# Kernel optimization log

Hardware: AMD Instinct MI355X
Metric: run time of the kernel (lower is better)

Reference implementation:

```python
import jax, jax.numpy as jnp
import numpy as np

B, N = 256, 100000

def setup_inputs() -> dict:
    key = jax.random.key(0)
    k1, k2 = jax.random.split(key)
    preds = jax.random.normal(k1, (B, N), dtype=jnp.float32)
    labels = jax.random.normal(k2, (B, N), dtype=jnp.float32)
    return {"preds": preds, "labels": labels, "subject": 0}

def reference(preds, labels, subject):
    # Batch-parallel Pearson: five fused row reductions instead of a Python loop.
    n = jnp.asarray(preds.shape[1], preds.dtype)
    sum_x = jnp.sum(preds, axis=1)
    sum_y = jnp.sum(labels, axis=1)
    sum_xy = jnp.sum(preds * labels, axis=1)
    sum_x2 = jnp.sum(preds * preds, axis=1)
    sum_y2 = jnp.sum(labels * labels, axis=1)
    num = n * sum_xy - sum_x * sum_y
    den = jnp.sqrt((n * sum_x2 - sum_x ** 2) * (n * sum_y2 - sum_y ** 2))
    pearson = num / den
    return jnp.mean(1.0 - pearson)
```

## Files before the change

kernel.cpp:

```cpp
#include <hip/hip_runtime.h>

#define B_ROWS   256
#define SPLIT    8
#define NTHREADS 256
#define NBLOCKS  (B_ROWS * SPLIT)


__global__ __launch_bounds__(NTHREADS) void pearson_partial(
    const float* __restrict__ preds,
    const float* __restrict__ labels,
    float* __restrict__ ws,
    int N)
{
    const int bid = blockIdx.x;
    const int row = bid >> 3;
    const int seg = bid & (SPLIT - 1);
    const int tid = threadIdx.x;

    const int n4      = N >> 2;
    const int per_seg = n4 / SPLIT;
    const int begin   = seg * per_seg;
    const int end     = begin + per_seg;

    const float4* p4 = reinterpret_cast<const float4*>(preds  + (size_t)row * N);
    const float4* l4 = reinterpret_cast<const float4*>(labels + (size_t)row * N);

    float sx = 0.f, sy = 0.f, sxy = 0.f, sxx = 0.f, syy = 0.f;

    for (int i = begin + tid; i < end; i += NTHREADS) {
        float4 a = p4[i];
        float4 b = l4[i];
        sx += a.x; sy += b.x; sxy = fmaf(a.x, b.x, sxy); sxx = fmaf(a.x, a.x, sxx); syy = fmaf(b.x, b.x, syy);
        sx += a.y; sy += b.y; sxy = fmaf(a.y, b.y, sxy); sxx = fmaf(a.y, a.y, sxx); syy = fmaf(b.y, b.y, syy);
        sx += a.z; sy += b.z; sxy = fmaf(a.z, b.z, sxy); sxx = fmaf(a.z, a.z, sxx); syy = fmaf(b.z, b.z, syy);
        sx += a.w; sy += b.w; sxy = fmaf(a.w, b.w, sxy); sxx = fmaf(a.w, a.w, sxx); syy = fmaf(b.w, b.w, syy);
    }

    for (int o = 32; o > 0; o >>= 1) {
        sx  += __shfl_down(sx,  o, 64);
        sy  += __shfl_down(sy,  o, 64);
        sxy += __shfl_down(sxy, o, 64);
        sxx += __shfl_down(sxx, o, 64);
        syy += __shfl_down(syy, o, 64);
    }

    __shared__ float red[4][5];
    const int wave = tid >> 6;
    const int lane = tid & 63;
    if (lane == 0) {
        red[wave][0] = sx;  red[wave][1] = sy;  red[wave][2] = sxy;
        red[wave][3] = sxx; red[wave][4] = syy;
    }
    __syncthreads();

    if (tid == 0) {
        ws[0 * NBLOCKS + bid] = red[0][0] + red[1][0] + red[2][0] + red[3][0];
        ws[1 * NBLOCKS + bid] = red[0][1] + red[1][1] + red[2][1] + red[3][1];
        ws[2 * NBLOCKS + bid] = red[0][2] + red[1][2] + red[2][2] + red[3][2];
        ws[3 * NBLOCKS + bid] = red[0][3] + red[1][3] + red[2][3] + red[3][3];
        ws[4 * NBLOCKS + bid] = red[0][4] + red[1][4] + red[2][4] + red[3][4];
    }
}

__global__ __launch_bounds__(NTHREADS) void pearson_final(
    const float* __restrict__ ws,
    float* __restrict__ out,
    int N)
{
    const int t = threadIdx.x;
    const float4* ws4 = reinterpret_cast<const float4*>(ws);

    float4 v[5][2];
#pragma unroll
    for (int j = 0; j < 5; ++j) {
        v[j][0] = ws4[j * (NBLOCKS / 4) + 2 * t];
        v[j][1] = ws4[j * (NBLOCKS / 4) + 2 * t + 1];
    }

    double acc[5];
#pragma unroll
    for (int j = 0; j < 5; ++j) {
        acc[j] = (double)v[j][0].x + (double)v[j][0].y + (double)v[j][0].z + (double)v[j][0].w
               + (double)v[j][1].x + (double)v[j][1].y + (double)v[j][1].z + (double)v[j][1].w;
    }

    const double n   = (double)N;
    const double num = n * acc[2] - acc[0] * acc[1];
    const double den = sqrt((n * acc[3] - acc[0] * acc[0]) * (n * acc[4] - acc[1] * acc[1]));
    double val = 1.0 - num / den;

    for (int o = 32; o > 0; o >>= 1)
        val += __shfl_down(val, o, 64);

    __shared__ double dred[4];
    const int wave = t >> 6;
    const int lane = t & 63;
    if (lane == 0) dred[wave] = val;
    __syncthreads();

    if (t == 0)
        out[0] = (float)((dred[0] + dred[1] + dred[2] + dred[3]) / (double)B_ROWS);
}

extern "C" void kernel_launch(void* const* d_in, const int* in_sizes, int n_in,
                              void* d_out, int out_size, void* d_ws, size_t ws_size,
                              hipStream_t stream)
{
    const float* preds  = (const float*)d_in[0];
    const float* labels = (const float*)d_in[1];

    const int N = in_sizes[0] / B_ROWS;

    float* ws  = (float*)d_ws;
    float* out = (float*)d_out;

    pearson_partial<<<NBLOCKS, NTHREADS, 0, stream>>>(preds, labels, ws, N);
    pearson_final<<<1, NTHREADS, 0, stream>>>(ws, out, N);
}
```

Measured before the change: 37.82 us.

## Fuse partial and final Pearson kernels into one row-per-block kernel with atomic output

Replaces the two-kernel scheme (8 blocks per row writing partials, then a single-block final reduction) with one kernel. Each 1024-thread block reduces a full row, computes that row's Pearson term in double, and atomically adds it into the output, which is zeroed by a memset. This removes the second launch and the workspace round-trip. In exchange only 256 blocks cover the GPU, which may underfill the CUs for a bandwidth-bound stream, and the float atomic summation order is nondeterministic.

```diff
diff --git a/kernel.cpp b/kernel.cpp
--- a/kernel.cpp
+++ b/kernel.cpp
@@ -1,35 +1,39 @@
 #include <hip/hip_runtime.h>
 
-#define B_ROWS   256
-#define SPLIT    8
-#define NTHREADS 256
-#define NBLOCKS  (B_ROWS * SPLIT)
+#define B_ROWS 256
+#define NT     1024
 
-
-__global__ __launch_bounds__(NTHREADS) void pearson_partial(
+__global__ __launch_bounds__(NT) void pearson_row(
     const float* __restrict__ preds,
     const float* __restrict__ labels,
-    float* __restrict__ ws,
+    float* __restrict__ out,
     int N)
 {
-    const int bid = blockIdx.x;
-    const int row = bid >> 3;
-    const int seg = bid & (SPLIT - 1);
+    const int row = blockIdx.x;
     const int tid = threadIdx.x;
 
-    const int n4      = N >> 2;
-    const int per_seg = n4 / SPLIT;
-    const int begin   = seg * per_seg;
-    const int end     = begin + per_seg;
+    const int n4   = N >> 2;
+    const int full = n4 / NT;
+    const int rem  = n4 - full * NT;
 
     const float4* p4 = reinterpret_cast<const float4*>(preds  + (size_t)row * N);
     const float4* l4 = reinterpret_cast<const float4*>(labels + (size_t)row * N);
 
     float sx = 0.f, sy = 0.f, sxy = 0.f, sxx = 0.f, syy = 0.f;
 
-    for (int i = begin + tid; i < end; i += NTHREADS) {
+    int i = tid;
+#pragma unroll 4
+    for (int k = 0; k < full; ++k, i += NT) {
         float4 a = p4[i];
         float4 b = l4[i];
+        sx += a.x; sy += b.x; sxy = fmaf(a.x, b.x, sxy); sxx = fmaf(a.x, a.x, sxx); syy = fmaf(b.x, b.x, syy);
+        sx += a.y; sy += b.y; sxy = fmaf(a.y, b.y, sxy); sxx = fmaf(a.y, a.y, sxx); syy = fmaf(b.y, b.y, syy);
+        sx += a.z; sy += b.z; sxy = fmaf(a.z, b.z, sxy); sxx = fmaf(a.z, a.z, sxx); syy = fmaf(b.z, b.z, syy);
+        sx += a.w; sy += b.w; sxy = fmaf(a.w, b.w, sxy); sxx = fmaf(a.w, a.w, sxx); syy = fmaf(b.w, b.w, syy);
+    }
+    if (tid < rem) {
+        float4 a = p4[full * NT + tid];
+        float4 b = l4[full * NT + tid];
         sx += a.x; sy += b.x; sxy = fmaf(a.x, b.x, sxy); sxx = fmaf(a.x, a.x, sxx); syy = fmaf(b.x, b.x, syy);
         sx += a.y; sy += b.y; sxy = fmaf(a.y, b.y, sxy); sxx = fmaf(a.y, a.y, sxx); syy = fmaf(b.y, b.y, syy);
         sx += a.z; sy += b.z; sxy = fmaf(a.z, b.z, sxy); sxx = fmaf(a.z, a.z, sxx); syy = fmaf(b.z, b.z, syy);
@@ -44,7 +48,7 @@
         syy += __shfl_down(syy, o, 64);
     }
 
-    __shared__ float red[4][5];
+    __shared__ float red[NT / 64][5];
     const int wave = tid >> 6;
     const int lane = tid & 63;
     if (lane == 0) {
@@ -54,52 +58,21 @@
     __syncthreads();
 
     if (tid == 0) {
-        ws[0 * NBLOCKS + bid] = red[0][0] + red[1][0] + red[2][0] + red[3][0];
-        ws[1 * NBLOCKS + bid] = red[0][1] + red[1][1] + red[2][1] + red[3][1];
-        ws[2 * NBLOCKS + bid] = red[0][2] + red[1][2] + red[2][2] + red[3][2];
-        ws[3 * NBLOCKS + bid] = red[0][3] + red[1][3] + red[2][3] + red[3][3];
-        ws[4 * NBLOCKS + bid] = red[0][4] + red[1][4] + red[2][4] + red[3][4];
+        double acc0 = 0.0, acc1 = 0.0, acc2 = 0.0, acc3 = 0.0, acc4 = 0.0;
+#pragma unroll
+        for (int w = 0; w < NT / 64; ++w) {
+            acc0 += (double)red[w][0];
+            acc1 += (double)red[w][1];
+            acc2 += (double)red[w][2];
+            acc3 += (double)red[w][3];
+            acc4 += (double)red[w][4];
+        }
+        const double n   = (double)N;
+        const double num = n * acc2 - acc0 * acc1;
+        const double den = sqrt((n * acc3 - acc0 * acc0) * (n * acc4 - acc1 * acc1));
+        const double val = (1.0 - num / den) / (double)B_ROWS;
+        atomicAdd(out, (float)val);
     }
-}
-
-__global__ __launch_bounds__(NTHREADS) void pearson_final(
-    const float* __restrict__ ws,
-    float* __restrict__ out,
-    int N)
-{
-    const int t = threadIdx.x;
-    const float4* ws4 = reinterpret_cast<const float4*>(ws);
-
-    float4 v[5][2];
-#pragma unroll
-    for (int j = 0; j < 5; ++j) {
-        v[j][0] = ws4[j * (NBLOCKS / 4) + 2 * t];
-        v[j][1] = ws4[j * (NBLOCKS / 4) + 2 * t + 1];
-    }
-
-    double acc[5];
-#pragma unroll
-    for (int j = 0; j < 5; ++j) {
-        acc[j] = (double)v[j][0].x + (double)v[j][0].y + (double)v[j][0].z + (double)v[j][0].w
-               + (double)v[j][1].x + (double)v[j][1].y + (double)v[j][1].z + (double)v[j][1].w;
-    }
-
-    const double n   = (double)N;
-    const double num = n * acc[2] - acc[0] * acc[1];
-    const double den = sqrt((n * acc[3] - acc[0] * acc[0]) * (n * acc[4] - acc[1] * acc[1]));
-    double val = 1.0 - num / den;
-
-    for (int o = 32; o > 0; o >>= 1)
-        val += __shfl_down(val, o, 64);
-
-    __shared__ double dred[4];
-    const int wave = t >> 6;
-    const int lane = t & 63;
-    if (lane == 0) dred[wave] = val;
-    __syncthreads();
-
-    if (t == 0)
-        out[0] = (float)((dred[0] + dred[1] + dred[2] + dred[3]) / (double)B_ROWS);
 }
 
 extern "C" void kernel_launch(void* const* d_in, const int* in_sizes, int n_in,
@@ -110,10 +83,8 @@
     const float* labels = (const float*)d_in[1];
 
     const int N = in_sizes[0] / B_ROWS;
-
-    float* ws  = (float*)d_ws;
     float* out = (float*)d_out;
 
-    pearson_partial<<<NBLOCKS, NTHREADS, 0, stream>>>(preds, labels, ws, N);
-    pearson_final<<<1, NTHREADS, 0, stream>>>(ws, out, N);
+    hipMemsetAsync(out, 0, sizeof(float), stream);
+    pearson_row<<<B_ROWS, NT, 0, stream>>>(preds, labels, out, N);
 }
```

Result: slower. 40.49 us (+7.1%).
